# Kernel tuning notes

Measured on AMD Instinct MI355X. Metric: run time of the kernel, lower is better.

The kernel has to match this reference:

```python
import jax, jax.numpy as jnp
import numpy as np

R_UNIT = 0.1
C_UNIT = 0.2
SCALE_FACTOR = 1.0
DBU = 2000.0
NUM_NETS = 200000
NET_SIZE = 16
N_PINS = NUM_NETS * NET_SIZE
BU_ITERS = NET_SIZE   # tree depth <= 15 < NET_SIZE, fixed-point converges
TD_JUMPS = 5          # pointer doubling: covers path length 2^5-1 >= 15


def setup_inputs() -> dict:
    key = jax.random.key(0)
    k1, k2, k3, k4, k5 = jax.random.split(key, 5)
    rng = np.random.default_rng(0)
    # per-net random tree: local pin 0 is root (fa = self), pin i has parent in [0, i)
    fa_local = np.floor(rng.random((NUM_NETS, NET_SIZE)) * np.arange(NET_SIZE)).astype(np.int32)
    offs = (np.arange(NUM_NETS, dtype=np.int32) * NET_SIZE)[:, None]
    pin_fa = (fa_local + offs).reshape(-1)
    is_child = (np.tile(np.arange(NET_SIZE), (NUM_NETS, 1)) > 0).reshape(-1)
    flat_pin_to = np.arange(N_PINS, dtype=np.int32)[is_child]
    flat_pin_from = pin_fa[is_child]
    order = np.argsort(flat_pin_from, kind='stable')  # children CSR sorted by parent
    flat_pin_from = np.ascontiguousarray(flat_pin_from[order])
    flat_pin_to = np.ascontiguousarray(flat_pin_to[order])
    flat_pin_to_start = np.searchsorted(flat_pin_from, np.arange(N_PINS + 1)).astype(np.int32)
    net_flat_topo_sort = np.arange(N_PINS, dtype=np.int32)
    net_flat_topo_sort_start = np.arange(NUM_NETS + 1, dtype=np.int32) * NET_SIZE
    return {
        'new_x': jax.random.uniform(k1, (N_PINS,), jnp.float32, 0.0, 1e6),
        'new_y': jax.random.uniform(k2, (N_PINS,), jnp.float32, 0.0, 1e6),
        'net_flat_topo_sort': jnp.asarray(net_flat_topo_sort),
        'net_flat_topo_sort_start': jnp.asarray(net_flat_topo_sort_start),
        'pin_fa': jnp.asarray(pin_fa),
        'flat_pin_to_start': jnp.asarray(flat_pin_to_start),
        'flat_pin_to': jnp.asarray(flat_pin_to),
        'flat_pin_from': jnp.asarray(flat_pin_from),
        'pin_caps_base': jax.random.uniform(k3, (N_PINS,), jnp.float32, 0.5, 2.0),
        'pin_rcaps_base': jax.random.uniform(k4, (N_PINS,), jnp.float32, 0.5, 2.0),
        'pin_fcaps_base': jax.random.uniform(k5, (N_PINS,), jnp.float32, 0.5, 2.0),
    }


def _subtree_sum(base, fa, not_root, n_iter=BU_ITERS):
    # Bottom-up: out[i] = base[i] + sum_{c: fa[c]=i} out[c]  (Load / LDelay recurrences)
    def body(_, acc):
        child = jnp.zeros_like(acc).at[fa].add(jnp.where(not_root, acc, 0.0))
        return base + child
    return jax.lax.fori_loop(0, n_iter, body, base)


def _path_sum(x, fa, n_jump=TD_JUMPS):
    # Top-down: out[i] = out[fa[i]] + x[i], root (fa=self, x=0) -> parallel pointer jumping
    def body(_, carry):
        s, p = carry
        return (s + s[p], p[p])
    s, _ = jax.lax.fori_loop(0, n_jump, body, (x, fa))
    return s


def reference(new_x, new_y, net_flat_topo_sort, net_flat_topo_sort_start, pin_fa,
              flat_pin_to_start, flat_pin_to, flat_pin_from,
              pin_caps_base, pin_rcaps_base, pin_fcaps_base):
    length = (jnp.abs(new_x[flat_pin_from] - new_x[flat_pin_to])
              + jnp.abs(new_y[flat_pin_from] - new_y[flat_pin_to])) / SCALE_FACTOR / DBU
    cap_e = length * C_UNIT
    net_caps = (jnp.zeros_like(new_x)
                .at[flat_pin_from].add(cap_e * 0.5)
                .at[flat_pin_to].add(cap_e * 0.5))
    res_e = length * R_UNIT
    res_pin = jnp.zeros_like(new_x).at[flat_pin_to].set(res_e)  # 0 at roots
    not_root = pin_fa != jnp.arange(new_x.shape[0], dtype=pin_fa.dtype)

    def mode(base_cap):
        pin_cap = base_cap + net_caps
        load = _subtree_sum(pin_cap, pin_fa, not_root)            # Load = Cap + sum(children)
        delay = _path_sum(res_pin * load, pin_fa)                 # Delay = Delay(fa) + R*Load
        ldelay = _subtree_sum(pin_cap * delay, pin_fa, not_root)  # LDelay = C*Delay + sum(children)
        beta = _path_sum(res_pin * ldelay, pin_fa)                # Beta = Beta(fa) + R*LDelay
        impulse = jnp.sqrt(jnp.clip(2.0 * beta - delay * delay, 1e-12))
        return jnp.stack([pin_cap, load, delay, ldelay, beta, impulse])  # [6, N]

    # [6 outputs, 3 modes (generic, rise, fall), N pins]
    return jnp.stack([mode(pin_caps_base), mode(pin_rcaps_base), mode(pin_fcaps_base)], axis=1)
```

## Files before the change

kernel.cpp:

```cpp
#include <hip/hip_runtime.h>
#include <math.h>


namespace {
constexpr int NS = 16;
constexpr int BLOCK = 64;
constexpr int ST = 17;
constexpr float INV_DBU = 1.0f / 2000.0f;
}

#define FA(j) ((int)((((j) < 8 ? p0 : p1) >> (((j) & 7) * 4)) & 15u))

__global__ __launch_bounds__(BLOCK) void rc_timing_kernel(
    const float* __restrict__ gx, const float* __restrict__ gy,
    const int* __restrict__ gfa,
    const float* __restrict__ base0, const float* __restrict__ base1,
    const float* __restrict__ base2,
    float* __restrict__ out, int n_pins)
{
  __shared__ float sA[BLOCK * ST];
  __shared__ float sB[BLOCK * ST];
  __shared__ float sC[BLOCK * ST];
  __shared__ float sD[BLOCK * ST];

  const int t = threadIdx.x;
  const int pinbase = blockIdx.x * (BLOCK * NS);
  if (pinbase >= n_pins) return;
  const int row = t * ST;

  auto coopload = [&](const float* __restrict__ g, float* s) {
#pragma unroll
    for (int k = 0; k < 4; ++k) {
      const int f = k * (BLOCK * 4) + t * 4;
      const float4 v = *reinterpret_cast<const float4*>(g + f);
      float* p = s + (f >> 4) * ST + (f & 15);
      p[0] = v.x; p[1] = v.y; p[2] = v.z; p[3] = v.w;
    }
  };
  auto coopstore = [&](const float* s, float* __restrict__ g) {
#pragma unroll
    for (int k = 0; k < 4; ++k) {
      const int f = k * (BLOCK * 4) + t * 4;
      const float* p = s + (f >> 4) * ST + (f & 15);
      *reinterpret_cast<float4*>(g + f) = make_float4(p[0], p[1], p[2], p[3]);
    }
  };

  unsigned p0, p1;
  {
    const int* f = gfa + pinbase + t * NS;
    const int4 a = *reinterpret_cast<const int4*>(f + 0);
    const int4 b = *reinterpret_cast<const int4*>(f + 4);
    const int4 c = *reinterpret_cast<const int4*>(f + 8);
    const int4 d = *reinterpret_cast<const int4*>(f + 12);
    const int off = pinbase + t * NS;
    p0 = (unsigned)(a.x - off)        | ((unsigned)(a.y - off) << 4)  |
         ((unsigned)(a.z - off) << 8) | ((unsigned)(a.w - off) << 12) |
         ((unsigned)(b.x - off) << 16)| ((unsigned)(b.y - off) << 20) |
         ((unsigned)(b.z - off) << 24)| ((unsigned)(b.w - off) << 28);
    p1 = (unsigned)(c.x - off)        | ((unsigned)(c.y - off) << 4)  |
         ((unsigned)(c.z - off) << 8) | ((unsigned)(c.w - off) << 12) |
         ((unsigned)(d.x - off) << 16)| ((unsigned)(d.y - off) << 20) |
         ((unsigned)(d.z - off) << 24)| ((unsigned)(d.w - off) << 28);
  }

  coopload(gx + pinbase, sA);
  coopload(gy + pinbase, sB);
#pragma unroll
  for (int j = 0; j < NS; ++j) sC[row + j] = 0.0f;
  __syncthreads();

  float res[NS];
  res[0] = 0.0f;
#pragma unroll
  for (int i = 1; i < NS; ++i) {
    const int fa = FA(i);
    const float dx = fabsf(sA[row + fa] - sA[row + i]);
    const float dy = fabsf(sB[row + fa] - sB[row + i]);
    const float len = (dx + dy) * INV_DBU;
    const float r = len * 0.1f;
    res[i] = r;
    sC[row + i] += r;
    sC[row + fa] += r;
  }
  __syncthreads();

#pragma unroll 1
  for (int m = 0; m < 3; ++m) {
    const float* bp = (m == 0) ? base0 : ((m == 1) ? base1 : base2);
    coopload(bp + pinbase, sA);
    __syncthreads();

#pragma unroll
    for (int j = 0; j < NS; ++j) sA[row + j] += sC[row + j];
    __syncthreads();
    coopstore(sA, out + (size_t)(0 * 3 + m) * n_pins + pinbase);

#pragma unroll
    for (int j = 0; j < NS; ++j) sB[row + j] = sA[row + j];
#pragma unroll
    for (int i = NS - 1; i >= 1; --i) sB[row + FA(i)] += sB[row + i];
    __syncthreads();
    coopstore(sB, out + (size_t)(1 * 3 + m) * n_pins + pinbase);

    sD[row + 0] = 0.0f;
#pragma unroll
    for (int i = 1; i < NS; ++i)
      sD[row + i] = sD[row + FA(i)] + res[i] * sB[row + i];
    __syncthreads();
    coopstore(sD, out + (size_t)(2 * 3 + m) * n_pins + pinbase);

#pragma unroll
    for (int j = 0; j < NS; ++j) sB[row + j] = sA[row + j] * sD[row + j];
#pragma unroll
    for (int i = NS - 1; i >= 1; --i) sB[row + FA(i)] += sB[row + i];
    __syncthreads();
    coopstore(sB, out + (size_t)(3 * 3 + m) * n_pins + pinbase);

    sA[row + 0] = 0.0f;
#pragma unroll
    for (int i = 1; i < NS; ++i)
      sA[row + i] = sA[row + FA(i)] + res[i] * sB[row + i];
    __syncthreads();
    coopstore(sA, out + (size_t)(4 * 3 + m) * n_pins + pinbase);

#pragma unroll
    for (int j = 0; j < NS; ++j) {
      const float bb = sA[row + j];
      const float dd = sD[row + j];
      sB[row + j] = sqrtf(fmaxf(2.0f * bb - dd * dd, 1e-12f));
    }
    __syncthreads();
    coopstore(sB, out + (size_t)(5 * 3 + m) * n_pins + pinbase);
    __syncthreads();
  }
}

extern "C" void kernel_launch(void* const* d_in, const int* in_sizes, int n_in,
                              void* d_out, int out_size, void* d_ws, size_t ws_size,
                              hipStream_t stream) {
  const float* gx = (const float*)d_in[0];
  const float* gy = (const float*)d_in[1];
  const int*   gfa = (const int*)d_in[4];
  const float* b0 = (const float*)d_in[8];
  const float* b1 = (const float*)d_in[9];
  const float* b2 = (const float*)d_in[10];
  float* out = (float*)d_out;

  const int n_pins = in_sizes[0];
  const int nets = n_pins / NS;
  const int grid = (nets + BLOCK - 1) / BLOCK;
  rc_timing_kernel<<<grid, BLOCK, 0, stream>>>(gx, gy, gfa, b0, b1, b2, out,
                                               n_pins);
}
```

Before: 336.2 us.

## Process all three cap modes together in registers and shared memory

Replaces the serial loop over the three capacitance modes with one pass that handles generic, rise and fall at once. It uses three shared arrays, one per mode, and keeps the pin caps and delays in registers, cutting the shared-memory footprint and interleaving independent dependency chains for more ILP. The extra register arrays (P, D, c) raise register pressure, which may force spills or lower occupancy.

```diff
diff --git a/kernel.cpp b/kernel.cpp
--- a/kernel.cpp
+++ b/kernel.cpp
@@ -18,14 +18,12 @@
     const float* __restrict__ base2,
     float* __restrict__ out, int n_pins)
 {
-  __shared__ float sA[BLOCK * ST];
-  __shared__ float sB[BLOCK * ST];
-  __shared__ float sC[BLOCK * ST];
-  __shared__ float sD[BLOCK * ST];
+  __shared__ float s0[BLOCK * ST];
+  __shared__ float s1[BLOCK * ST];
+  __shared__ float s2[BLOCK * ST];
 
   const int t = threadIdx.x;
   const int pinbase = blockIdx.x * (BLOCK * NS);
-  if (pinbase >= n_pins) return;
   const int row = t * ST;
 
   auto coopload = [&](const float* __restrict__ g, float* s) {
@@ -51,23 +49,23 @@
     const int* f = gfa + pinbase + t * NS;
     const int4 a = *reinterpret_cast<const int4*>(f + 0);
     const int4 b = *reinterpret_cast<const int4*>(f + 4);
-    const int4 c = *reinterpret_cast<const int4*>(f + 8);
-    const int4 d = *reinterpret_cast<const int4*>(f + 12);
+    const int4 c4 = *reinterpret_cast<const int4*>(f + 8);
+    const int4 d4 = *reinterpret_cast<const int4*>(f + 12);
     const int off = pinbase + t * NS;
-    p0 = (unsigned)(a.x - off)        | ((unsigned)(a.y - off) << 4)  |
-         ((unsigned)(a.z - off) << 8) | ((unsigned)(a.w - off) << 12) |
-         ((unsigned)(b.x - off) << 16)| ((unsigned)(b.y - off) << 20) |
-         ((unsigned)(b.z - off) << 24)| ((unsigned)(b.w - off) << 28);
-    p1 = (unsigned)(c.x - off)        | ((unsigned)(c.y - off) << 4)  |
-         ((unsigned)(c.z - off) << 8) | ((unsigned)(c.w - off) << 12) |
-         ((unsigned)(d.x - off) << 16)| ((unsigned)(d.y - off) << 20) |
-         ((unsigned)(d.z - off) << 24)| ((unsigned)(d.w - off) << 28);
-  }
-
-  coopload(gx + pinbase, sA);
-  coopload(gy + pinbase, sB);
-#pragma unroll
-  for (int j = 0; j < NS; ++j) sC[row + j] = 0.0f;
+    p0 = (unsigned)(a.x - off)         | ((unsigned)(a.y - off) << 4)  |
+         ((unsigned)(a.z - off) << 8)  | ((unsigned)(a.w - off) << 12) |
+         ((unsigned)(b.x - off) << 16) | ((unsigned)(b.y - off) << 20) |
+         ((unsigned)(b.z - off) << 24) | ((unsigned)(b.w - off) << 28);
+    p1 = (unsigned)(c4.x - off)        | ((unsigned)(c4.y - off) << 4)  |
+         ((unsigned)(c4.z - off) << 8) | ((unsigned)(c4.w - off) << 12) |
+         ((unsigned)(d4.x - off) << 16)| ((unsigned)(d4.y - off) << 20) |
+         ((unsigned)(d4.z - off) << 24)| ((unsigned)(d4.w - off) << 28);
+  }
+
+  coopload(gx + pinbase, s0);
+  coopload(gy + pinbase, s1);
+#pragma unroll
+  for (int j = 0; j < NS; ++j) s2[row + j] = 0.0f;
   __syncthreads();
 
   float res[NS];
@@ -75,65 +73,113 @@
 #pragma unroll
   for (int i = 1; i < NS; ++i) {
     const int fa = FA(i);
-    const float dx = fabsf(sA[row + fa] - sA[row + i]);
-    const float dy = fabsf(sB[row + fa] - sB[row + i]);
-    const float len = (dx + dy) * INV_DBU;
-    const float r = len * 0.1f;
+    const float dx = fabsf(s0[row + fa] - s0[row + i]);
+    const float dy = fabsf(s1[row + fa] - s1[row + i]);
+    const float r = (dx + dy) * (INV_DBU * 0.1f);
     res[i] = r;
-    sC[row + i] += r;
-    sC[row + fa] += r;
-  }
-  __syncthreads();
-
-#pragma unroll 1
-  for (int m = 0; m < 3; ++m) {
-    const float* bp = (m == 0) ? base0 : ((m == 1) ? base1 : base2);
-    coopload(bp + pinbase, sA);
-    __syncthreads();
-
-#pragma unroll
-    for (int j = 0; j < NS; ++j) sA[row + j] += sC[row + j];
-    __syncthreads();
-    coopstore(sA, out + (size_t)(0 * 3 + m) * n_pins + pinbase);
-
-#pragma unroll
-    for (int j = 0; j < NS; ++j) sB[row + j] = sA[row + j];
-#pragma unroll
-    for (int i = NS - 1; i >= 1; --i) sB[row + FA(i)] += sB[row + i];
-    __syncthreads();
-    coopstore(sB, out + (size_t)(1 * 3 + m) * n_pins + pinbase);
-
-    sD[row + 0] = 0.0f;
-#pragma unroll
-    for (int i = 1; i < NS; ++i)
-      sD[row + i] = sD[row + FA(i)] + res[i] * sB[row + i];
-    __syncthreads();
-    coopstore(sD, out + (size_t)(2 * 3 + m) * n_pins + pinbase);
-
-#pragma unroll
-    for (int j = 0; j < NS; ++j) sB[row + j] = sA[row + j] * sD[row + j];
-#pragma unroll
-    for (int i = NS - 1; i >= 1; --i) sB[row + FA(i)] += sB[row + i];
-    __syncthreads();
-    coopstore(sB, out + (size_t)(3 * 3 + m) * n_pins + pinbase);
-
-    sA[row + 0] = 0.0f;
-#pragma unroll
-    for (int i = 1; i < NS; ++i)
-      sA[row + i] = sA[row + FA(i)] + res[i] * sB[row + i];
-    __syncthreads();
-    coopstore(sA, out + (size_t)(4 * 3 + m) * n_pins + pinbase);
-
-#pragma unroll
-    for (int j = 0; j < NS; ++j) {
-      const float bb = sA[row + j];
-      const float dd = sD[row + j];
-      sB[row + j] = sqrtf(fmaxf(2.0f * bb - dd * dd, 1e-12f));
-    }
-    __syncthreads();
-    coopstore(sB, out + (size_t)(5 * 3 + m) * n_pins + pinbase);
-    __syncthreads();
-  }
+    s2[row + i] += r;
+    s2[row + fa] += r;
+  }
+  float c[NS];
+#pragma unroll
+  for (int j = 0; j < NS; ++j) c[j] = s2[row + j];
+  __syncthreads();
+
+  coopload(base0 + pinbase, s0);
+  coopload(base1 + pinbase, s1);
+  coopload(base2 + pinbase, s2);
+  __syncthreads();
+
+  float P[3][NS];
+#pragma unroll
+  for (int j = 0; j < NS; ++j) {
+    P[0][j] = s0[row + j] + c[j]; s0[row + j] = P[0][j];
+    P[1][j] = s1[row + j] + c[j]; s1[row + j] = P[1][j];
+    P[2][j] = s2[row + j] + c[j]; s2[row + j] = P[2][j];
+  }
+  __syncthreads();
+  coopstore(s0, out + (size_t)0 * n_pins + pinbase);
+  coopstore(s1, out + (size_t)1 * n_pins + pinbase);
+  coopstore(s2, out + (size_t)2 * n_pins + pinbase);
+  __syncthreads();
+
+#pragma unroll
+  for (int i = NS - 1; i >= 1; --i) {
+    const int fa = FA(i);
+    const float a0 = s0[row + i], a1 = s1[row + i], a2 = s2[row + i];
+    s0[row + fa] += a0;
+    s1[row + fa] += a1;
+    s2[row + fa] += a2;
+  }
+  __syncthreads();
+  coopstore(s0, out + (size_t)3 * n_pins + pinbase);
+  coopstore(s1, out + (size_t)4 * n_pins + pinbase);
+  coopstore(s2, out + (size_t)5 * n_pins + pinbase);
+  __syncthreads();
+
+  s0[row] = 0.0f; s1[row] = 0.0f; s2[row] = 0.0f;
+#pragma unroll
+  for (int i = 1; i < NS; ++i) {
+    const int fa = FA(i);
+    s0[row + i] = s0[row + fa] + res[i] * s0[row + i];
+    s1[row + i] = s1[row + fa] + res[i] * s1[row + i];
+    s2[row + i] = s2[row + fa] + res[i] * s2[row + i];
+  }
+  __syncthreads();
+  coopstore(s0, out + (size_t)6 * n_pins + pinbase);
+  coopstore(s1, out + (size_t)7 * n_pins + pinbase);
+  coopstore(s2, out + (size_t)8 * n_pins + pinbase);
+  float D[3][NS];
+#pragma unroll
+  for (int j = 0; j < NS; ++j) {
+    D[0][j] = s0[row + j]; D[1][j] = s1[row + j]; D[2][j] = s2[row + j];
+  }
+  __syncthreads();
+
+#pragma unroll
+  for (int j = 0; j < NS; ++j) {
+    s0[row + j] = P[0][j] * D[0][j];
+    s1[row + j] = P[1][j] * D[1][j];
+    s2[row + j] = P[2][j] * D[2][j];
+  }
+#pragma unroll
+  for (int i = NS - 1; i >= 1; --i) {
+    const int fa = FA(i);
+    const float a0 = s0[row + i], a1 = s1[row + i], a2 = s2[row + i];
+    s0[row + fa] += a0;
+    s1[row + fa] += a1;
+    s2[row + fa] += a2;
+  }
+  __syncthreads();
+  coopstore(s0, out + (size_t)9  * n_pins + pinbase);
+  coopstore(s1, out + (size_t)10 * n_pins + pinbase);
+  coopstore(s2, out + (size_t)11 * n_pins + pinbase);
+  __syncthreads();
+
+  s0[row] = 0.0f; s1[row] = 0.0f; s2[row] = 0.0f;
+#pragma unroll
+  for (int i = 1; i < NS; ++i) {
+    const int fa = FA(i);
+    s0[row + i] = s0[row + fa] + res[i] * s0[row + i];
+    s1[row + i] = s1[row + fa] + res[i] * s1[row + i];
+    s2[row + i] = s2[row + fa] + res[i] * s2[row + i];
+  }
+  __syncthreads();
+  coopstore(s0, out + (size_t)12 * n_pins + pinbase);
+  coopstore(s1, out + (size_t)13 * n_pins + pinbase);
+  coopstore(s2, out + (size_t)14 * n_pins + pinbase);
+  __syncthreads();
+
+#pragma unroll
+  for (int j = 0; j < NS; ++j) {
+    s0[row + j] = sqrtf(fmaxf(2.0f * s0[row + j] - D[0][j] * D[0][j], 1e-12f));
+    s1[row + j] = sqrtf(fmaxf(2.0f * s1[row + j] - D[1][j] * D[1][j], 1e-12f));
+    s2[row + j] = sqrtf(fmaxf(2.0f * s2[row + j] - D[2][j] * D[2][j], 1e-12f));
+  }
+  __syncthreads();
+  coopstore(s0, out + (size_t)15 * n_pins + pinbase);
+  coopstore(s1, out + (size_t)16 * n_pins + pinbase);
+  coopstore(s2, out + (size_t)17 * n_pins + pinbase);
 }
 
 extern "C" void kernel_launch(void* const* d_in, const int* in_sizes, int n_in,
```

After: 332.9 us. About the same (-1.0%).
